# Kernel tuning notes

Measured on AMD Instinct MI355X. Metric: run time of the kernel, lower is better.

Reference implementation:

```python
import jax, jax.numpy as jnp
import numpy as np

N_NODES = 50000
N_EDGES = 800000
BATCH = 128
D_IN = 768
D_H = 256
EPS_BN = 1e-5
EPS_COS = 1e-8


def setup_inputs() -> dict:
    key = jax.random.key(0)
    ks = jax.random.split(key, 16)
    s = 0.05
    return {
        "claim_embeddings": jax.random.normal(ks[0], (BATCH, D_IN), jnp.float32),
        "x": jax.random.normal(ks[1], (N_NODES, D_IN), jnp.float32),
        "edge_index": jax.random.randint(ks[2], (2, N_EDGES), 0, N_NODES, jnp.int32),
        "batch": jnp.sort(jax.random.randint(ks[3], (N_NODES,), 0, BATCH, jnp.int32)),
        "W1": jax.random.normal(ks[4], (D_IN, D_H), jnp.float32) * s,
        "a_src1": jax.random.normal(ks[5], (D_H,), jnp.float32) * s,
        "a_dst1": jax.random.normal(ks[6], (D_H,), jnp.float32) * s,
        "b1": jnp.zeros((D_H,), jnp.float32),
        "W2": jax.random.normal(ks[7], (D_H, D_H), jnp.float32) * s,
        "a_src2": jax.random.normal(ks[8], (D_H,), jnp.float32) * s,
        "a_dst2": jax.random.normal(ks[9], (D_H,), jnp.float32) * s,
        "b2": jnp.zeros((D_H,), jnp.float32),
        "bn_gamma": jnp.ones((D_H,), jnp.float32),
        "bn_beta": jnp.zeros((D_H,), jnp.float32),
        "Wc": jax.random.normal(ks[10], (D_H + D_IN, 1), jnp.float32) * s,
        "bc": jnp.zeros((1,), jnp.float32),
    }


def _gat_layer(h_in, src, dst, W, a_s, a_d, b, n_nodes):
    """PyG GATConv (heads=1, concat=True, self-loops already in src/dst)."""
    h = h_in @ W                                   # [N, D_H]
    alpha_s = h @ a_s                               # [N]
    alpha_d = h @ a_d                               # [N]
    e = jax.nn.leaky_relu(alpha_s[src] + alpha_d[dst], 0.2)  # [E+N]
    # numerically-stable softmax segmented by destination node
    e = e - jax.ops.segment_max(e, dst, num_segments=n_nodes)[dst]
    w = jnp.exp(e)
    w = w / jax.ops.segment_sum(w, dst, num_segments=n_nodes)[dst]
    out = jax.ops.segment_sum(h[src] * w[:, None], dst, num_segments=n_nodes)
    return out + b


def reference(claim_embeddings, x, edge_index, batch,
              W1, a_src1, a_dst1, b1, W2, a_src2, a_dst2, b2,
              bn_gamma, bn_beta, Wc, bc):
    n = x.shape[0]
    n_graphs = claim_embeddings.shape[0]
    # cosine-similarity relevance gating (torch eps semantics)
    ce = claim_embeddings[batch]                    # [N, D_IN]
    denom = jnp.maximum(jnp.linalg.norm(ce, axis=-1) * jnp.linalg.norm(x, axis=-1), EPS_COS)
    rel = jnp.sum(ce * x, axis=-1) / denom          # [N]
    h = x * rel[:, None]
    # add self-loops once (GATConv default add_self_loops=True)
    loops = jnp.arange(n, dtype=edge_index.dtype)
    src = jnp.concatenate([edge_index[0], loops])
    dst = jnp.concatenate([edge_index[1], loops])
    # layer 1 + batchnorm (batch stats) + relu
    h = _gat_layer(h, src, dst, W1, a_src1, a_dst1, b1, n)
    mean = jnp.mean(h, axis=0)
    var = jnp.mean(jnp.square(h - mean), axis=0)
    h = bn_gamma * (h - mean) * jax.lax.rsqrt(var + EPS_BN) + bn_beta
    h = jax.nn.relu(h)
    # layer 2 + relu
    h = _gat_layer(h, src, dst, W2, a_src2, a_dst2, b2, n)
    h = jax.nn.relu(h)
    # global mean pool per graph
    sums = jax.ops.segment_sum(h, batch, num_segments=n_graphs)
    counts = jax.ops.segment_sum(jnp.ones((n,), h.dtype), batch, num_segments=n_graphs)
    pooled = sums / jnp.maximum(counts, 1.0)[:, None]   # [B, D_H]
    combined = jnp.concatenate([pooled, claim_embeddings], axis=1)  # [B, D_H+D_IN]
    out = combined @ Wc + bc                        # [B, 1]
    return out.squeeze(-1)
```

## Files before the change

kernel.cpp:

```cpp
#include <hip/hip_runtime.h>
#include <hip/hip_bf16.h>

#define DIN 768
#define DH  256

typedef unsigned short ushort_t;
typedef __attribute__((ext_vector_type(8))) short short8v;
typedef __attribute__((ext_vector_type(4))) float f32x4;

__host__ __device__ inline int orig_col(int s) {
  return (s & ~63) | (s & 0x20) | ((s & 1) << 4) | ((s >> 1) & 0xF);
}

__device__ inline float wave_sum(float v) {
#pragma unroll
  for (int o = 32; o; o >>= 1) v += __shfl_xor(v, o);
  return v;
}
__device__ inline void wave_sum2(float& a, float& b) {
#pragma unroll
  for (int o = 32; o; o >>= 1) {
    a += __shfl_xor(a, o);
    b += __shfl_xor(b, o);
  }
}
__device__ inline float leaky(float v) { return v > 0.f ? v : 0.2f * v; }

__device__ inline ushort_t f2bf(float f) {
  union { float f; unsigned u; } v; v.f = f;
  unsigned r = v.u + 0x7FFFu + ((v.u >> 16) & 1u);
  return (ushort_t)(r >> 16);
}
__device__ inline float bf2f(ushort_t u) {
  union { unsigned u; float f; } t; t.u = ((unsigned)u) << 16; return t.f;
}

__device__ inline void unpack8(uint4 v, float* f) {
  union { unsigned u; float f; } t;
  t.u = v.x << 16;         f[0] = t.f;
  t.u = v.x & 0xFFFF0000u; f[1] = t.f;
  t.u = v.y << 16;         f[2] = t.f;
  t.u = v.y & 0xFFFF0000u; f[3] = t.f;
  t.u = v.z << 16;         f[4] = t.f;
  t.u = v.z & 0xFFFF0000u; f[5] = t.f;
  t.u = v.w << 16;         f[6] = t.f;
  t.u = v.w & 0xFFFF0000u; f[7] = t.f;
}
__device__ inline uint4 pack8(const float* f) {
  uint4 o;
  o.x = (unsigned)f2bf(f[0]) | ((unsigned)f2bf(f[1]) << 16);
  o.y = (unsigned)f2bf(f[2]) | ((unsigned)f2bf(f[3]) << 16);
  o.z = (unsigned)f2bf(f[4]) | ((unsigned)f2bf(f[5]) << 16);
  o.w = (unsigned)f2bf(f[6]) | ((unsigned)f2bf(f[7]) << 16);
  return o;
}

__global__ __launch_bounds__(256) void relxb_hist_kernel(
    const float* __restrict__ ce, const float* __restrict__ x,
    const int* __restrict__ batch, const float* __restrict__ cenorm,
    ushort_t* __restrict__ xb, float* __restrict__ rel, int n,
    const int* __restrict__ edst, int E, int* __restrict__ cnt) {
  int node = blockIdx.x * 4 + (threadIdx.x >> 6);
  int lane = threadIdx.x & 63;
  if (node < n) {
    int g = batch[node];
    const float4* xr = (const float4*)(x + (size_t)node * DIN);
    const float4* cr = (const float4*)(ce + (size_t)g * DIN);
    float dxy = 0.f, dxx = 0.f;
#pragma unroll
    for (int i = 0; i < 3; i++) {
      float4 a = xr[lane + 64 * i];
      float4 b = cr[lane + 64 * i];
      ushort4 o = make_ushort4(f2bf(a.x), f2bf(a.y), f2bf(a.z), f2bf(a.w));
      *(ushort4*)&xb[(size_t)node * DIN + (lane + 64 * i) * 4] = o;
      dxy += a.x*b.x + a.y*b.y + a.z*b.z + a.w*b.w;
      dxx += a.x*a.x + a.y*a.y + a.z*a.z + a.w*a.w;
    }
    wave_sum2(dxy, dxx);
    if (lane == 0) {
      float denom = fmaxf(sqrtf(dxx) * cenorm[g], 1e-8f);
      rel[node] = dxy / denom;
    }
  }
  for (int e = blockIdx.x * blockDim.x + threadIdx.x; e < E;
       e += gridDim.x * blockDim.x)
    atomicAdd(&cnt[edst[e]], 1);
}

__global__ __launch_bounds__(256) void prep_kernel(
    const float* __restrict__ W1, const float* __restrict__ W2,
    const float* __restrict__ b1, const float* __restrict__ b2,
    const float* __restrict__ gamma, const float* __restrict__ beta,
    const float* __restrict__ Wc, const float* __restrict__ ce,
    ushort_t* __restrict__ Wt1, ushort_t* __restrict__ Wt2,
    float* __restrict__ pb1, float* __restrict__ pb2,
    float* __restrict__ pgamma, float* __restrict__ pbeta,
    float* __restrict__ pWc, float* __restrict__ cenorm, int B) {
  __shared__ float tile[64][65];
  int b = blockIdx.x;
  int t = threadIdx.x;
  int r4 = t >> 6;
  int c64 = t & 63;
  if (b < 48) {
    int k0 = (b % 12) * 64, c0 = (b / 12) * 64;
#pragma unroll
    for (int rr = 0; rr < 16; rr++) {
      int r = rr * 4 + r4;
      tile[r][c64] = W1[(size_t)(k0 + r) * 256 + c0 + c64];
    }
    __syncthreads();
#pragma unroll
    for (int rr = 0; rr < 16; rr++) {
      int cc = rr * 4 + r4;
      Wt1[(size_t)(c0 + cc) * DIN + k0 + c64] = f2bf(tile[c64][cc]);
    }
  } else if (b < 64) {
    int bb = b - 48;
    int k0 = (bb & 3) * 64, c0 = (bb >> 2) * 64;
#pragma unroll
    for (int rr = 0; rr < 16; rr++) {
      int r = rr * 4 + r4;
      tile[r][c64] = W2[(size_t)orig_col(k0 + r) * 256 + c0 + c64];
    }
    __syncthreads();
#pragma unroll
    for (int rr = 0; rr < 16; rr++) {
      int cc = rr * 4 + r4;
      Wt2[(size_t)(c0 + cc) * DH + k0 + c64] = f2bf(tile[c64][cc]);
    }
  } else if (b == 64) {
    int o = orig_col(t);
    pb1[t] = b1[o];
    pb2[t] = b2[o];
    pgamma[t] = gamma[o];
    pbeta[t] = beta[o];
    pWc[t] = Wc[o];
  } else {
    int lane = t & 63;
    for (int g = r4; g < B; g += 4) {
      const float4* cr = (const float4*)(ce + (size_t)g * DIN);
      float s = 0.f;
#pragma unroll
      for (int i = 0; i < 3; i++) {
        float4 v = cr[lane + 64 * i];
        s += v.x*v.x + v.y*v.y + v.z*v.z + v.w*v.w;
      }
      s = wave_sum(s);
      if (lane == 0) cenorm[g] = sqrtf(s);
    }
  }
}

__global__ __launch_bounds__(256) void scan1_kernel(const int* __restrict__ cnt,
                                                    int* __restrict__ row_off,
                                                    int* __restrict__ bsum, int n) {
  __shared__ int s[256];
  int t = threadIdx.x;
  int i = blockIdx.x * 256 + t;
  int v = (i < n) ? cnt[i] : 0;
  s[t] = v;
  __syncthreads();
  for (int off = 1; off < 256; off <<= 1) {
    int tmp = (t >= off) ? s[t - off] : 0;
    __syncthreads();
    s[t] += tmp;
    __syncthreads();
  }
  if (i < n) row_off[i] = s[t] - v;
  if (t == 255) bsum[blockIdx.x] = s[255];
}

__global__ __launch_bounds__(256) void scan2_kernel(const int* __restrict__ bsum,
                                                    int* __restrict__ boff, int nb,
                                                    int* __restrict__ row_off, int n) {
  __shared__ int s[256];
  int t = threadIdx.x;
  int v = (t < nb) ? bsum[t] : 0;
  s[t] = v;
  __syncthreads();
  for (int off = 1; off < 256; off <<= 1) {
    int tmp = (t >= off) ? s[t - off] : 0;
    __syncthreads();
    s[t] += tmp;
    __syncthreads();
  }
  if (t < nb) boff[t] = s[t] - v;
  if (t == nb - 1) row_off[n] = s[t];
}

__global__ __launch_bounds__(256) void scan3_kernel(int* __restrict__ row_off,
                                                    const int* __restrict__ boff, int n) {
  int i = blockIdx.x * 256 + threadIdx.x;
  if (i < n) row_off[i] += boff[blockIdx.x];
}

__global__ void fill_kernel(const int* __restrict__ src, const int* __restrict__ dst, int E,
                            const int* __restrict__ row_off, int* __restrict__ fill,
                            int* __restrict__ col_src) {
  for (int e = blockIdx.x * blockDim.x + threadIdx.x; e < E; e += gridDim.x * blockDim.x) {
    int d = dst[e];
    int slot = row_off[d] + atomicAdd(&fill[d], 1);
    col_src[slot] = src[e];
  }
}

template <int K>
__global__ __launch_bounds__(256) void gemm_mfma(
    const ushort_t* __restrict__ A, const ushort_t* __restrict__ Bt,
    ushort_t* __restrict__ C, const float* __restrict__ scale,
    const float* __restrict__ a_s, const float* __restrict__ a_d,
    float* __restrict__ alpha_s, float* __restrict__ alpha_d, int Mreal) {
  __shared__ ushort_t lds[16384];
  const int tid = threadIdx.x;
  const int lane = tid & 63;
  const int wave = tid >> 6;

  int p = blockIdx.y * 2 + blockIdx.x;
  int total = 2 * gridDim.y;
  int cch = p >> 4;
  int v;
  if ((cch << 4) + 16 <= total) {
    int r = p & 15;
    v = (cch << 4) | ((r & 7) << 1) | (r >> 3);
  } else {
    v = p;
  }
  const int col0 = (v & 1) * 128;
  const int row0 = (v >> 1) * 128;

  const int wr = wave >> 1, wc = wave & 1;
  const int c16 = lane & 15, g4 = lane >> 4;
  const int st_roff = lane >> 3;
  const int st_gsrc = (lane & 7) ^ st_roff;

  f32x4 acc[4][4];
#pragma unroll
  for (int m = 0; m < 4; m++)
#pragma unroll
    for (int nn = 0; nn < 4; nn++)
#pragma unroll
      for (int j = 0; j < 4; j++) acc[m][nn][j] = 0.f;

  for (int k0 = 0; k0 < K; k0 += 64) {
#pragma unroll
    for (int ci = 0; ci < 8; ci++) {
      int inst = wave * 8 + ci;
      int isB = inst >> 4;
      int idx = inst & 15;
      int lrow = idx * 8 + st_roff;
      const ushort_t* gsrc;
      if (isB == 0) {
        int rg = row0 + lrow;
        rg = rg < Mreal ? rg : Mreal - 1;
        gsrc = A + (size_t)rg * K + k0 + st_gsrc * 8;
      } else {
        gsrc = Bt + (size_t)(col0 + lrow) * K + k0 + st_gsrc * 8;
      }
      __builtin_amdgcn_global_load_lds(
          (const __attribute__((address_space(1))) void*)gsrc,
          (__attribute__((address_space(3))) void*)&lds[isB * 8192 + idx * 512],
          16, 0, 0);
    }
    __syncthreads();
#pragma unroll
    for (int ks = 0; ks < 2; ks++) {
      int g = ks * 4 + g4;
      short8v a[4], b[4];
#pragma unroll
      for (int m = 0; m < 4; m++) {
        int ra = wr * 64 + m * 16 + c16;
        a[m] = *(const short8v*)&lds[ra * 64 + (g ^ (ra & 7)) * 8];
      }
#pragma unroll
      for (int nn = 0; nn < 4; nn++) {
        int rb = wc * 64 + nn * 16 + c16;
        b[nn] = *(const short8v*)&lds[8192 + rb * 64 + (g ^ (rb & 7)) * 8];
      }
#pragma unroll
      for (int m = 0; m < 4; m++)
#pragma unroll
        for (int nn = 0; nn < 4; nn++)
          acc[m][nn] = __builtin_amdgcn_mfma_f32_16x16x32_bf16(a[m], b[nn],
                                                               acc[m][nn], 0, 0, 0);
    }
    __syncthreads();
  }

  float asv[4], adv[4];
#pragma unroll
  for (int nn = 0; nn < 4; nn++) {
    int col = col0 + wc * 64 + nn * 16 + c16;
    asv[nn] = a_s[col];
    adv[nn] = a_d[col];
  }

  uint* Cw = (uint*)C;
#pragma unroll
  for (int m = 0; m < 4; m++) {
    int row_base = row0 + wr * 64 + m * 16 + g4 * 4;
#pragma unroll
    for (int j = 0; j < 4; j++) {
      int row = row_base + j;
      int rc = row < Mreal ? row : Mreal - 1;
      float s = scale ? scale[rc] : 1.0f;
      float vs[4];
      float ps = 0.f, pd = 0.f;
#pragma unroll
      for (int nn = 0; nn < 4; nn++) {
        float v2 = acc[m][nn][j] * s;
        vs[nn] = v2;
        ps = fmaf(v2, asv[nn], ps);
        pd = fmaf(v2, adv[nn], pd);
      }
#pragma unroll
      for (int o = 1; o < 16; o <<= 1) {
        ps += __shfl_xor(ps, o);
        pd += __shfl_xor(pd, o);
      }
      if (c16 == 0 && row < Mreal) {
        atomicAdd(&alpha_s[row], ps);
        atomicAdd(&alpha_d[row], pd);
      }
      if (row < Mreal) {
#pragma unroll
        for (int q = 0; q < 2; q++) {
          unsigned wv = (unsigned)f2bf(vs[2 * q]) |
                        ((unsigned)f2bf(vs[2 * q + 1]) << 16);
          Cw[(size_t)row * 128 + (col0 >> 1) + wc * 32 + q * 16 + c16] = wv;
        }
      }
    }
  }
}

__global__ __launch_bounds__(256) void gat_agg(
    const ushort_t* __restrict__ hb, const float* __restrict__ as_,
    const float* __restrict__ ad_, const int* __restrict__ row_off,
    const int* __restrict__ col_src, const float* __restrict__ bias,
    ushort_t* __restrict__ outb, int n, int relu_out) {
  int node = blockIdx.x * 4 + (threadIdx.x >> 6);
  int lane = threadIdx.x & 63;
  if (node >= n) return;
  int lo = row_off[node], hi = row_off[node + 1];
  int deg = hi - lo;
  float adn = ad_[node];
  float w_self = __expf(leaky(as_[node] + adn));

  const int q = lane >> 4;
  const int l16 = lane & 15;
  const ushort_t* rowbase = hb + (size_t)l16 * 16;

  float acc[16];
  float zacc = (lane == 0) ? w_self : 0.f;
  {
    const uint4* ps = (const uint4*)(rowbase + (size_t)node * 256);
    uint4 v0 = ps[0], v1 = ps[1];
    float ws = (q == 0) ? w_self : 0.f;
    float f[16];
    unpack8(v0, f);
    unpack8(v1, f + 8);
#pragma unroll
    for (int i = 0; i < 16; i++) acc[i] = ws * f[i];
  }

  for (int base = 0; base < deg; base += 64) {
    int cnt = min(64, deg - base);
    int s = 0; float w = 0.f;
    if (lane < cnt) {
      s = col_src[lo + base + lane];
      w = __expf(leaky(as_[s] + adn));
    }
    zacc += w;
    int e = 0;
    for (; e + 8 <= cnt; e += 8) {
      int iA = e + q, iB = e + 4 + q;
      int sA = __shfl(s, iA);
      float wA = __shfl(w, iA);
      int sB = __shfl(s, iB);
      float wB = __shfl(w, iB);
      const uint4* pA = (const uint4*)(rowbase + (size_t)sA * 256);
      const uint4* pB = (const uint4*)(rowbase + (size_t)sB * 256);
      uint4 a0 = pA[0], a1 = pA[1];
      uint4 b0 = pB[0], b1 = pB[1];
      float f[16];
      unpack8(a0, f);
      unpack8(a1, f + 8);
#pragma unroll
      for (int i = 0; i < 16; i++) acc[i] = fmaf(wA, f[i], acc[i]);
      unpack8(b0, f);
      unpack8(b1, f + 8);
#pragma unroll
      for (int i = 0; i < 16; i++) acc[i] = fmaf(wB, f[i], acc[i]);
    }
    for (; e < cnt; e += 4) {
      int myE = e + q;
      int idx = myE < cnt ? myE : cnt - 1;
      int ss = __shfl(s, idx);
      float wv = __shfl(w, idx);
      float wgt = (myE < cnt) ? wv : 0.f;
      const uint4* pp = (const uint4*)(rowbase + (size_t)ss * 256);
      uint4 v0 = pp[0], v1 = pp[1];
      float f[16];
      unpack8(v0, f);
      unpack8(v1, f + 8);
#pragma unroll
      for (int i = 0; i < 16; i++) acc[i] = fmaf(wgt, f[i], acc[i]);
    }
  }

  float z = wave_sum(zacc);
  float inv_z = 1.0f / z;

#pragma unroll
  for (int i = 0; i < 16; i++) {
    acc[i] += __shfl_xor(acc[i], 16);
    acc[i] += __shfl_xor(acc[i], 32);
  }

  if (q == 0) {
    float o[16];
#pragma unroll
    for (int i = 0; i < 16; i += 4) {
      float4 bb = *(const float4*)&bias[l16 * 16 + i];
      o[i]     = fmaf(acc[i],     inv_z, bb.x);
      o[i + 1] = fmaf(acc[i + 1], inv_z, bb.y);
      o[i + 2] = fmaf(acc[i + 2], inv_z, bb.z);
      o[i + 3] = fmaf(acc[i + 3], inv_z, bb.w);
    }
    if (relu_out) {
#pragma unroll
      for (int i = 0; i < 16; i++) o[i] = fmaxf(o[i], 0.f);
    }
    uint4* op = (uint4*)(outb + (size_t)node * 256 + l16 * 16);
    op[0] = pack8(o);
    op[1] = pack8(o + 8);
  }
}

__global__ __launch_bounds__(256) void bn_stats(const ushort_t* __restrict__ h, int n,
                                                float* __restrict__ bsum,
                                                float* __restrict__ bsq) {
  int c = threadIdx.x;
  int rows_per_block = (n + gridDim.x - 1) / gridDim.x;
  int r0 = blockIdx.x * rows_per_block;
  int r1 = min(r0 + rows_per_block, n);
  float sum = 0.f, sq = 0.f;
  for (int r = r0; r < r1; r++) {
    float v = bf2f(h[(size_t)r * 256 + c]);
    sum += v;
    sq = fmaf(v, v, sq);
  }
  atomicAdd(&bsum[c], sum);
  atomicAdd(&bsq[c], sq);
}

__global__ __launch_bounds__(256) void bn_apply(const ushort_t* __restrict__ h,
                                                const float* __restrict__ bsum,
                                                const float* __restrict__ bsq,
                                                const float* __restrict__ gamma,
                                                const float* __restrict__ beta,
                                                ushort_t* __restrict__ h2b, int n) {
  int total4 = n * 64;
  float inv_n = 1.0f / (float)n;
  for (int f = blockIdx.x * blockDim.x + threadIdx.x; f < total4;
       f += gridDim.x * blockDim.x) {
    int c4 = f & 63;
    uint2 hv = ((const uint2*)h)[f];
    float v0, v1, v2, v3;
    {
      union { unsigned u; float fl; } t;
      t.u = hv.x << 16;         v0 = t.fl;
      t.u = hv.x & 0xFFFF0000u; v1 = t.fl;
      t.u = hv.y << 16;         v2 = t.fl;
      t.u = hv.y & 0xFFFF0000u; v3 = t.fl;
    }
    float4 sm = ((const float4*)bsum)[c4];
    float4 sl = ((const float4*)bsq)[c4];
    float4 g = ((const float4*)gamma)[c4];
    float4 bb = ((const float4*)beta)[c4];
    float m, var;
    m = sm.x * inv_n; var = sl.x * inv_n - m * m;
    v0 = fmaxf(g.x * (v0 - m) * rsqrtf(var + 1e-5f) + bb.x, 0.f);
    m = sm.y * inv_n; var = sl.y * inv_n - m * m;
    v1 = fmaxf(g.y * (v1 - m) * rsqrtf(var + 1e-5f) + bb.y, 0.f);
    m = sm.z * inv_n; var = sl.z * inv_n - m * m;
    v2 = fmaxf(g.z * (v2 - m) * rsqrtf(var + 1e-5f) + bb.z, 0.f);
    m = sm.w * inv_n; var = sl.w * inv_n - m * m;
    v3 = fmaxf(g.w * (v3 - m) * rsqrtf(var + 1e-5f) + bb.w, 0.f);
    uint2 o;
    o.x = (unsigned)f2bf(v0) | ((unsigned)f2bf(v1) << 16);
    o.y = (unsigned)f2bf(v2) | ((unsigned)f2bf(v3) << 16);
    ((uint2*)h2b)[f] = o;
  }
}

__device__ inline int lower_bound_dev(const int* a, int n, int v) {
  int lo = 0, hi = n;
  while (lo < hi) {
    int mid = (lo + hi) >> 1;
    if (a[mid] < v) lo = mid + 1; else hi = mid;
  }
  return lo;
}

#define POOL_CHUNKS 16
__global__ __launch_bounds__(256) void pool_partial(const ushort_t* __restrict__ h,
                                                    const int* __restrict__ batch, int n,
                                                    float* __restrict__ psum) {
  int g = blockIdx.x / POOL_CHUNKS;
  int c = blockIdx.x % POOL_CHUNKS;
  int lo = lower_bound_dev(batch, n, g);
  int hi = lower_bound_dev(batch, n, g + 1);
  int len = hi - lo;
  int r0 = lo + (int)(((long long)len * c) / POOL_CHUNKS);
  int r1 = lo + (int)(((long long)len * (c + 1)) / POOL_CHUNKS);
  if (r1 <= r0) return;
  float sum = 0.f;
  for (int r = r0; r < r1; r++) sum += bf2f(h[(size_t)r * 256 + threadIdx.x]);
  atomicAdd(&psum[(size_t)g * 256 + threadIdx.x], sum);
}

__global__ __launch_bounds__(256) void final_kernel(const float* __restrict__ psum,
                                                    const int* __restrict__ batch, int n,
                                                    const float* __restrict__ ce,
                                                    const float* __restrict__ pWc,
                                                    const float* __restrict__ Wc,
                                                    const float* __restrict__ bc,
                                                    float* __restrict__ out, int B) {
  int g = blockIdx.x;
  int t = threadIdx.x;
  int lo = lower_bound_dev(batch, n, g);
  int hi = lower_bound_dev(batch, n, g + 1);
  float inv_cnt = 1.0f / fmaxf((float)(hi - lo), 1.0f);
  float p = 0.f;
  p = fmaf(psum[(size_t)g * 256 + t] * inv_cnt, pWc[t], p);
  p = fmaf(ce[(size_t)g * 768 + t],        Wc[256 + t], p);
  p = fmaf(ce[(size_t)g * 768 + 256 + t],  Wc[512 + t], p);
  p = fmaf(ce[(size_t)g * 768 + 512 + t],  Wc[768 + t], p);
  __shared__ float red[256];
  red[t] = p;
  __syncthreads();
  for (int s = 128; s; s >>= 1) {
    if (t < s) red[t] += red[t + s];
    __syncthreads();
  }
  if (t == 0) out[g] = red[0] + bc[0];
}

extern "C" void kernel_launch(void* const* d_in, const int* in_sizes, int n_in,
                              void* d_out, int out_size, void* d_ws, size_t ws_size,
                              hipStream_t stream) {
  const float* ce    = (const float*)d_in[0];
  const float* x     = (const float*)d_in[1];
  const int*   edge  = (const int*)d_in[2];
  const int*   batch = (const int*)d_in[3];
  const float* W1    = (const float*)d_in[4];
  const float* a_s1  = (const float*)d_in[5];
  const float* a_d1  = (const float*)d_in[6];
  const float* b1    = (const float*)d_in[7];
  const float* W2    = (const float*)d_in[8];
  const float* a_s2  = (const float*)d_in[9];
  const float* a_d2  = (const float*)d_in[10];
  const float* b2    = (const float*)d_in[11];
  const float* gamma = (const float*)d_in[12];
  const float* beta  = (const float*)d_in[13];
  const float* Wc    = (const float*)d_in[14];
  const float* bc    = (const float*)d_in[15];

  const int B = in_sizes[0] / DIN;
  const int n = in_sizes[1] / DIN;
  const int E = in_sizes[2] / 2;
  const int* esrc = edge;
  const int* edst = edge + E;

  char* w = (char*)d_ws;
  size_t off = 0;
  auto carve = [&](size_t bytes) -> void* {
    void* p = w + off;
    off = (off + bytes + 255) & ~(size_t)255;
    return p;
  };
  size_t hbytes = (size_t)n * DH * 2;
  char*  R1      = (char*)carve((size_t)n * DIN * 2);
  ushort_t* xb    = (ushort_t*)R1;
  ushort_t* h1b   = (ushort_t*)R1;
  ushort_t* h2b   = (ushort_t*)(R1 + hbytes);
  ushort_t* buf_ob = (ushort_t*)(R1 + 2 * hbytes);
  ushort_t* buf_hb = (ushort_t*)carve(hbytes);
  int*   row_off = (int*)carve((size_t)(n + 1) * 4);
  int*   col_src = (int*)carve((size_t)E * 4);
  ushort_t* Wt1  = (ushort_t*)carve((size_t)DIN * DH * 2);
  ushort_t* Wt2  = (ushort_t*)carve((size_t)DH * DH * 2);
  float* pb1     = (float*)carve(DH * 4);
  float* pb2     = (float*)carve(DH * 4);
  float* pgamma  = (float*)carve(DH * 4);
  float* pbeta   = (float*)carve(DH * 4);
  float* pWc     = (float*)carve(DH * 4);
  float* cenorm  = (float*)carve((size_t)B * 4);
  float* rel     = (float*)carve((size_t)n * 4);
  int*   sc_bsum = (int*)carve(256 * 4);
  int*   sc_boff = (int*)carve(256 * 4);
  char* zero0 = (char*)carve((size_t)n * 4);
  int*   cnt     = (int*)zero0;
  int*   fill    = (int*)carve((size_t)n * 4);
  float* as1buf  = (float*)carve((size_t)n * 4);
  float* ad1buf  = (float*)carve((size_t)n * 4);
  float* as2buf  = (float*)carve((size_t)n * 4);
  float* ad2buf  = (float*)carve((size_t)n * 4);
  float* bn_sum  = (float*)carve(DH * 4);
  float* bn_sq   = (float*)carve(DH * 4);
  float* psum    = (float*)carve((size_t)B * DH * 4);
  size_t zero_bytes = (size_t)((char*)(psum + (size_t)B * DH) - zero0);

  hipMemsetAsync(zero0, 0, zero_bytes, stream);

  const int gN4 = (n + 3) / 4;
  const int Mb = (n + 127) / 128;
  const int nb = (n + 255) / 256;

  prep_kernel<<<66, 256, 0, stream>>>(W1, W2, b1, b2, gamma, beta, Wc, ce,
                                      Wt1, Wt2, pb1, pb2, pgamma, pbeta, pWc,
                                      cenorm, B);
  relxb_hist_kernel<<<gN4, 256, 0, stream>>>(ce, x, batch, cenorm, xb, rel, n,
                                             edst, E, cnt);
  scan1_kernel<<<nb, 256, 0, stream>>>(cnt, row_off, sc_bsum, n);
  scan2_kernel<<<1, 256, 0, stream>>>(sc_bsum, sc_boff, nb, row_off, n);
  scan3_kernel<<<nb, 256, 0, stream>>>(row_off, sc_boff, n);
  fill_kernel<<<1024, 256, 0, stream>>>(esrc, edst, E, row_off, fill, col_src);

  gemm_mfma<DIN><<<dim3(2, Mb), 256, 0, stream>>>(xb, Wt1, buf_hb, rel, a_s1,
                                                  a_d1, as1buf, ad1buf, n);
  gat_agg<<<gN4, 256, 0, stream>>>(buf_hb, as1buf, ad1buf, row_off, col_src, pb1,
                                   h1b, n, 0);
  bn_stats<<<512, 256, 0, stream>>>(h1b, n, bn_sum, bn_sq);
  bn_apply<<<2048, 256, 0, stream>>>(h1b, bn_sum, bn_sq, pgamma, pbeta, h2b, n);

  gemm_mfma<DH><<<dim3(2, Mb), 256, 0, stream>>>(h2b, Wt2, buf_hb, nullptr, a_s2,
                                                 a_d2, as2buf, ad2buf, n);
  gat_agg<<<gN4, 256, 0, stream>>>(buf_hb, as2buf, ad2buf, row_off, col_src, pb2,
                                   buf_ob, n, 1);

  pool_partial<<<B * POOL_CHUNKS, 256, 0, stream>>>(buf_ob, batch, n, psum);
  final_kernel<<<B, 256, 0, stream>>>(psum, batch, n, ce, pWc, Wc, bc,
                                      (float*)d_out, B);
}
```

Measured before the change: 417.8 us.

## Store projected GAT features in FP8 to halve gather traffic

After: 378.4 us (median of 2 runs). 9.4% less time.

```diff
diff --git a/kernel.cpp b/kernel.cpp
--- a/kernel.cpp
+++ b/kernel.cpp
@@ -5,11 +5,14 @@
 #define DH  256
 
 typedef unsigned short ushort_t;
+typedef unsigned char uchar_t;
 typedef __attribute__((ext_vector_type(8))) short short8v;
 typedef __attribute__((ext_vector_type(4))) float f32x4;
+typedef __attribute__((ext_vector_type(2))) float f32x2;
 
 __host__ __device__ inline int orig_col(int s) {
-  return (s & ~63) | (s & 0x20) | ((s & 1) << 4) | ((s >> 1) & 0xF);
+  int u = (s >> 2) & 31;
+  return (s & ~127) | (((u >> 4) & 1) << 6) | ((s & 3) << 4) | (u & 15);
 }
 
 __device__ inline float wave_sum(float v) {
@@ -35,16 +38,16 @@
   union { unsigned u; float f; } t; t.u = ((unsigned)u) << 16; return t.f;
 }
 
-__device__ inline void unpack8(uint4 v, float* f) {
-  union { unsigned u; float f; } t;
-  t.u = v.x << 16;         f[0] = t.f;
-  t.u = v.x & 0xFFFF0000u; f[1] = t.f;
-  t.u = v.y << 16;         f[2] = t.f;
-  t.u = v.y & 0xFFFF0000u; f[3] = t.f;
-  t.u = v.z << 16;         f[4] = t.f;
-  t.u = v.z & 0xFFFF0000u; f[5] = t.f;
-  t.u = v.w << 16;         f[6] = t.f;
-  t.u = v.w & 0xFFFF0000u; f[7] = t.f;
+__device__ inline void unpack16f8(uint4 v, float* f) {
+  f32x2 p;
+  p = __builtin_amdgcn_cvt_pk_f32_fp8(v.x, false); f[0] = p[0]; f[1] = p[1];
+  p = __builtin_amdgcn_cvt_pk_f32_fp8(v.x, true);  f[2] = p[0]; f[3] = p[1];
+  p = __builtin_amdgcn_cvt_pk_f32_fp8(v.y, false); f[4] = p[0]; f[5] = p[1];
+  p = __builtin_amdgcn_cvt_pk_f32_fp8(v.y, true);  f[6] = p[0]; f[7] = p[1];
+  p = __builtin_amdgcn_cvt_pk_f32_fp8(v.z, false); f[8] = p[0]; f[9] = p[1];
+  p = __builtin_amdgcn_cvt_pk_f32_fp8(v.z, true);  f[10] = p[0]; f[11] = p[1];
+  p = __builtin_amdgcn_cvt_pk_f32_fp8(v.w, false); f[12] = p[0]; f[13] = p[1];
+  p = __builtin_amdgcn_cvt_pk_f32_fp8(v.w, true);  f[14] = p[0]; f[15] = p[1];
 }
 __device__ inline uint4 pack8(const float* f) {
   uint4 o;
@@ -207,7 +210,7 @@
 template <int K>
 __global__ __launch_bounds__(256) void gemm_mfma(
     const ushort_t* __restrict__ A, const ushort_t* __restrict__ Bt,
-    ushort_t* __restrict__ C, const float* __restrict__ scale,
+    uchar_t* __restrict__ C, const float* __restrict__ scale,
     const float* __restrict__ a_s, const float* __restrict__ a_d,
     float* __restrict__ alpha_s, float* __restrict__ alpha_d, int Mreal) {
   __shared__ ushort_t lds[16384];
@@ -322,19 +325,16 @@
         atomicAdd(&alpha_d[row], pd);
       }
       if (row < Mreal) {
-#pragma unroll
-        for (int q = 0; q < 2; q++) {
-          unsigned wv = (unsigned)f2bf(vs[2 * q]) |
-                        ((unsigned)f2bf(vs[2 * q + 1]) << 16);
-          Cw[(size_t)row * 128 + (col0 >> 1) + wc * 32 + q * 16 + c16] = wv;
-        }
+        unsigned w8 = __builtin_amdgcn_cvt_pk_fp8_f32(vs[0], vs[1], 0u, false);
+        w8 = __builtin_amdgcn_cvt_pk_fp8_f32(vs[2], vs[3], w8, true);
+        Cw[(size_t)row * 64 + (col0 >> 2) + wc * 16 + c16] = w8;
       }
     }
   }
 }
 
 __global__ __launch_bounds__(256) void gat_agg(
-    const ushort_t* __restrict__ hb, const float* __restrict__ as_,
+    const uchar_t* __restrict__ h8, const float* __restrict__ as_,
     const float* __restrict__ ad_, const int* __restrict__ row_off,
     const int* __restrict__ col_src, const float* __restrict__ bias,
     ushort_t* __restrict__ outb, int n, int relu_out) {
@@ -348,17 +348,15 @@
 
   const int q = lane >> 4;
   const int l16 = lane & 15;
-  const ushort_t* rowbase = hb + (size_t)l16 * 16;
+  const uchar_t* rowbase = h8 + (size_t)l16 * 16;
 
   float acc[16];
   float zacc = (lane == 0) ? w_self : 0.f;
   {
-    const uint4* ps = (const uint4*)(rowbase + (size_t)node * 256);
-    uint4 v0 = ps[0], v1 = ps[1];
+    uint4 v = *(const uint4*)(rowbase + (size_t)node * 256);
     float ws = (q == 0) ? w_self : 0.f;
     float f[16];
-    unpack8(v0, f);
-    unpack8(v1, f + 8);
+    unpack16f8(v, f);
 #pragma unroll
     for (int i = 0; i < 16; i++) acc[i] = ws * f[i];
   }
@@ -378,17 +376,13 @@
       float wA = __shfl(w, iA);
       int sB = __shfl(s, iB);
       float wB = __shfl(w, iB);
-      const uint4* pA = (const uint4*)(rowbase + (size_t)sA * 256);
-      const uint4* pB = (const uint4*)(rowbase + (size_t)sB * 256);
-      uint4 a0 = pA[0], a1 = pA[1];
-      uint4 b0 = pB[0], b1 = pB[1];
+      uint4 a0 = *(const uint4*)(rowbase + (size_t)sA * 256);
+      uint4 b0 = *(const uint4*)(rowbase + (size_t)sB * 256);
       float f[16];
-      unpack8(a0, f);
-      unpack8(a1, f + 8);
+      unpack16f8(a0, f);
 #pragma unroll
       for (int i = 0; i < 16; i++) acc[i] = fmaf(wA, f[i], acc[i]);
-      unpack8(b0, f);
-      unpack8(b1, f + 8);
+      unpack16f8(b0, f);
 #pragma unroll
       for (int i = 0; i < 16; i++) acc[i] = fmaf(wB, f[i], acc[i]);
     }
@@ -398,11 +392,9 @@
       int ss = __shfl(s, idx);
       float wv = __shfl(w, idx);
       float wgt = (myE < cnt) ? wv : 0.f;
-      const uint4* pp = (const uint4*)(rowbase + (size_t)ss * 256);
-      uint4 v0 = pp[0], v1 = pp[1];
+      uint4 v = *(const uint4*)(rowbase + (size_t)ss * 256);
       float f[16];
-      unpack8(v0, f);
-      unpack8(v1, f + 8);
+      unpack16f8(v, f);
 #pragma unroll
       for (int i = 0; i < 16; i++) acc[i] = fmaf(wgt, f[i], acc[i]);
     }
@@ -580,13 +572,14 @@
     off = (off + bytes + 255) & ~(size_t)255;
     return p;
   };
-  size_t hbytes = (size_t)n * DH * 2;
+  size_t hbytes  = (size_t)n * DH * 2;
+  size_t h8bytes = (size_t)n * DH;
   char*  R1      = (char*)carve((size_t)n * DIN * 2);
   ushort_t* xb    = (ushort_t*)R1;
   ushort_t* h1b   = (ushort_t*)R1;
   ushort_t* h2b   = (ushort_t*)(R1 + hbytes);
   ushort_t* buf_ob = (ushort_t*)(R1 + 2 * hbytes);
-  ushort_t* buf_hb = (ushort_t*)carve(hbytes);
+  uchar_t* buf_h8 = (uchar_t*)carve(h8bytes);
   int*   row_off = (int*)carve((size_t)(n + 1) * 4);
   int*   col_src = (int*)carve((size_t)E * 4);
   ushort_t* Wt1  = (ushort_t*)carve((size_t)DIN * DH * 2);
@@ -628,16 +621,16 @@
   scan3_kernel<<<nb, 256, 0, stream>>>(row_off, sc_boff, n);
   fill_kernel<<<1024, 256, 0, stream>>>(esrc, edst, E, row_off, fill, col_src);
 
-  gemm_mfma<DIN><<<dim3(2, Mb), 256, 0, stream>>>(xb, Wt1, buf_hb, rel, a_s1,
+  gemm_mfma<DIN><<<dim3(2, Mb), 256, 0, stream>>>(xb, Wt1, buf_h8, rel, a_s1,
                                                   a_d1, as1buf, ad1buf, n);
-  gat_agg<<<gN4, 256, 0, stream>>>(buf_hb, as1buf, ad1buf, row_off, col_src, pb1,
+  gat_agg<<<gN4, 256, 0, stream>>>(buf_h8, as1buf, ad1buf, row_off, col_src, pb1,
                                    h1b, n, 0);
   bn_stats<<<512, 256, 0, stream>>>(h1b, n, bn_sum, bn_sq);
   bn_apply<<<2048, 256, 0, stream>>>(h1b, bn_sum, bn_sq, pgamma, pbeta, h2b, n);
 
-  gemm_mfma<DH><<<dim3(2, Mb), 256, 0, stream>>>(h2b, Wt2, buf_hb, nullptr, a_s2,
+  gemm_mfma<DH><<<dim3(2, Mb), 256, 0, stream>>>(h2b, Wt2, buf_h8, nullptr, a_s2,
                                                  a_d2, as2buf, ad2buf, n);
-  gat_agg<<<gN4, 256, 0, stream>>>(buf_hb, as2buf, ad2buf, row_off, col_src, pb2,
+  gat_agg<<<gN4, 256, 0, stream>>>(buf_h8, as2buf, ad2buf, row_off, col_src, pb2,
                                    buf_ob, n, 1);
 
   pool_partial<<<B * POOL_CHUNKS, 256, 0, stream>>>(buf_ob, batch, n, psum);
```
